# Optimization experiments

Measured on AMD Instinct MI355X. Metric: run time of the kernel, lower is better.

The kernel has to match this reference:

```python
import jax, jax.numpy as jnp
import numpy as np

B, N, H, HEADS, NBINS = 64, 256, 512, 8, 3
DK = H // HEADS
NEG = -1e12

def setup_inputs() -> dict:
    key = jax.random.key(0)
    ks = jax.random.split(key, 20)
    def lin(k, out_d, in_d):
        w = jax.random.normal(k, (out_d, in_d), jnp.float32) * (1.0 / np.sqrt(in_d))
        b = jnp.zeros((out_d,), jnp.float32)
        return w, b
    x = jax.random.normal(ks[0], (B, N, H), jnp.float32)
    dist = jax.random.uniform(ks[1], (B, N - 1, N - 1), jnp.float32, 0.0, 10.0)
    dist_bar = jnp.sort(jax.random.uniform(ks[2], (B, NBINS), jnp.float32, 1.0, 9.0), axis=-1)
    mask = jnp.ones((B, N, N), jnp.float32)
    Wq, bq = lin(ks[3], H, H)
    Wk, bk = lin(ks[4], H, H)
    Wv, bv = lin(ks[5], H, H)
    Wa = jnp.stack([lin(ks[6 + i], H, H)[0] for i in range(NBINS)])  # [NBINS,H,H]
    ba = jnp.zeros((NBINS, H), jnp.float32)
    Ws1, bs1 = lin(ks[10], H, NBINS * H)
    Ws2, bs2 = lin(ks[11], H, H)
    gamma = jnp.ones((H,), jnp.float32)
    beta = jnp.zeros((H,), jnp.float32)
    return dict(x=x, dist=dist, dist_bar=dist_bar, mask=mask, Wq=Wq, bq=bq, Wk=Wk, bk=bk,
                Wv=Wv, bv=bv, Wa=Wa, ba=ba, Ws1=Ws1, bs1=bs1, Ws2=Ws2, bs2=bs2,
                gamma=gamma, beta=beta)

def reference(x, dist, dist_bar, mask, Wq, bq, Wk, bk, Wv, bv, Wa, ba, Ws1, bs1, Ws2, bs2, gamma, beta):
    residual = x
    def proj(x, W, b):  # torch Linear: x @ W.T + b
        return jnp.einsum('bnd,od->bno', x, W) + b
    def heads(t):  # [B,N,H] -> [B,heads,N,dk]
        return t.reshape(B, N, HEADS, DK).transpose(0, 2, 1, 3)
    q, k, v = heads(proj(x, Wq, bq)), heads(proj(x, Wk, bk)), heads(proj(x, Wv, bv))
    scores = jnp.einsum('bhnd,bhmd->bhnm', q, k) / jnp.sqrt(jnp.float32(DK))  # [B,heads,N,N]
    # padding mask (shape [B,1,N,N] != scores shape -> masked_fill(mask==0))
    scores = jnp.where(mask[:, None] == 0, NEG, scores)
    # new_dist: super node row/col = 1, interior = dist
    new_dist = jnp.ones((B, 1, N, N), jnp.float32).at[:, :, 1:, 1:].set(dist[:, None])
    multi_out, attn_list = [], []
    for i in range(NBINS):
        cut = dist_bar[:, i][:, None, None, None]          # per-batch threshold
        dm = new_dist < cut                                 # [B,1,N,N]
        dm = dm.at[:, :, 0, :].set(True).at[:, :, :, 0].set(True)
        sd = jnp.where(dm, scores, NEG)
        attn = jax.nn.softmax(sd, axis=-1)                  # dropout: eval mode
        attn_list.append(attn)
        multi_out.append(jnp.einsum('bhnm,bhmd->bhnd', attn, v))
    x_cat = jnp.concatenate([
        jnp.einsum('bnd,od->bno', multi_out[i].transpose(0, 2, 1, 3).reshape(B, N, H), Wa[i]) + ba[i]
        for i in range(NBINS)], axis=-1)                    # [B,N,NBINS*H]
    h = jax.nn.silu(jnp.einsum('bnd,od->bno', x_cat, Ws1) + bs1)
    h = jnp.einsum('bnd,od->bno', h, Ws2) + bs2
    h = h + residual
    mu = jnp.mean(h, axis=-1, keepdims=True)
    var = jnp.var(h, axis=-1, keepdims=True)
    out = (h - mu) / jnp.sqrt(var + 1e-6) * gamma + beta
    return (out, jnp.stack(attn_list))
```

## Files before the change

### kernel.cpp

```cpp
#include <hip/hip_runtime.h>
#include <cstddef>

#define NEGV (-1e12f)


typedef __attribute__((ext_vector_type(4))) float f32x4;
typedef __attribute__((ext_vector_type(8))) __bf16 bf16x8;

__device__ __forceinline__ unsigned short f2bf(float f) {
  union { float f; unsigned u; } v; v.f = f;
  unsigned r = v.u + 0x7FFFu + ((v.u >> 16) & 1u);
  return (unsigned short)(r >> 16);
}

#define GLDS16(gp, lp)                                                      \
  __builtin_amdgcn_global_load_lds(                                         \
      (const __attribute__((address_space(1))) void*)(gp),                  \
      (__attribute__((address_space(3))) void*)(lp), 16, 0, 0)

__global__ __launch_bounds__(256) void msa_prep(
    const float* __restrict__ x, const float* __restrict__ Wq,
    const float* __restrict__ Wk, const float* __restrict__ Wv,
    const float* __restrict__ Ws2, const float* __restrict__ Ws1,
    const float* __restrict__ Wa, const float* __restrict__ bq,
    const float* __restrict__ bk, const float* __restrict__ bv,
    const float* __restrict__ ba, const float* __restrict__ bs1,
    const float* __restrict__ dist, const float* __restrict__ dist_bar,
    const float* __restrict__ maskg,
    unsigned short* __restrict__ xb, unsigned short* __restrict__ Wqkvb,
    unsigned short* __restrict__ Ws2b, unsigned short* __restrict__ Wcatb,
    float* __restrict__ bcomb, float* __restrict__ bqkv,
    unsigned long long* __restrict__ bits) {
  __shared__ float As[16][68];
  __shared__ float Bs[16][68];
  const int blk = blockIdx.x;
  const int tid = threadIdx.x;
  if (blk < 8192) {
    int i = blk * 256 + tid;
    float4 v = ((const float4*)x)[i];
    ushort4 o; o.x = f2bf(v.x); o.y = f2bf(v.y); o.z = f2bf(v.z); o.w = f2bf(v.w);
    ((ushort4*)xb)[i] = o;
    return;
  }
  if (blk < 8960) {
    int sel = (blk - 8192) >> 8;
    int i = ((blk - 8192) & 255) * 256 + tid;
    const float* src = (sel == 0) ? Wq : (sel == 1) ? Wk : Wv;
    unsigned short* dst = Wqkvb + (size_t)sel * 262144;
    float4 v = ((const float4*)src)[i];
    ushort4 o; o.x = f2bf(v.x); o.y = f2bf(v.y); o.z = f2bf(v.z); o.w = f2bf(v.w);
    ((ushort4*)dst)[i] = o;
    return;
  }
  if (blk < 9216) {
    int i = (blk - 8960) * 256 + tid;
    float4 v = ((const float4*)Ws2)[i];
    ushort4 o; o.x = f2bf(v.x); o.y = f2bf(v.y); o.z = f2bf(v.z); o.w = f2bf(v.w);
    ((ushort4*)Ws2b)[i] = o;
    return;
  }
  if (blk < 9408) {
    const int t = blk - 9216;
    const int i = t >> 6;
    const int ob = ((t >> 3) & 7) * 64, cb = (t & 7) * 64;
    const int tx = tid & 15, ty = tid >> 4;
    float acc[4][4] = {};
    for (int kt = 0; kt < 512; kt += 16) {
      __syncthreads();
      {
        int o = tid & 63, e4 = (tid >> 6) * 4;
        float4 a4 = *(const float4*)&Ws1[(size_t)(ob + o) * 1536 + i * 512 + kt + e4];
        As[e4 + 0][o] = a4.x; As[e4 + 1][o] = a4.y;
        As[e4 + 2][o] = a4.z; As[e4 + 3][o] = a4.w;
      }
      {
        int e = tid & 15, c4 = (tid >> 4) * 4;
        float4 b4 = *(const float4*)&Wa[((size_t)i << 18) + (size_t)(kt + e) * 512 + cb + c4];
        *(float4*)&Bs[e][c4] = b4;
      }
      __syncthreads();
#pragma unroll
      for (int k = 0; k < 16; ++k) {
        float a[4], bb[4];
        *(float4*)a = *(const float4*)&As[k][ty * 4];
        *(float4*)bb = *(const float4*)&Bs[k][tx * 4];
#pragma unroll
        for (int r = 0; r < 4; ++r)
#pragma unroll
          for (int c = 0; c < 4; ++c) acc[r][c] += a[r] * bb[c];
      }
    }
#pragma unroll
    for (int r = 0; r < 4; ++r)
#pragma unroll
      for (int c = 0; c < 4; ++c)
        Wcatb[(size_t)(ob + ty * 4 + r) * 1536 + i * 512 + cb + tx * 4 + c] =
            f2bf(acc[r][c]);
    return;
  }
  if (blk < 9410) {
    int o = (blk - 9408) * 256 + tid;
    float acc = bs1[o];
    for (int cidx = 0; cidx < 1536; ++cidx)
      acc += Ws1[(size_t)o * 1536 + cidx] * ba[cidx];
    bcomb[o] = acc;
    return;
  }
  if (blk < 9411) {
    for (int i = tid; i < 1536; i += 256)
      bqkv[i] = (i < 512) ? bq[i] : (i < 1024) ? bk[i - 512] : bv[i - 1024];
    return;
  }
  {
    const int gw = (blk - 9411) * 4 + (tid >> 6);
    const int lane = tid & 63;
    const int b = gw >> 8, row = gw & 255;
    const float cut0 = dist_bar[b * 3 + 0];
    const float cut1 = dist_bar[b * 3 + 1];
    const float cut2 = dist_bar[b * 3 + 2];
    const float* mrow = maskg + (size_t)b * 65536 + (size_t)row * 256;
    const int rj = (row == 0) ? 1 : row;
    const float* drow = dist + (size_t)b * 65025 + (size_t)(rj - 1) * 255;
    unsigned long long* out = bits + (size_t)gw * 12;
#pragma unroll
    for (int cc = 0; cc < 4; ++cc) {
      const int col = cc * 64 + lane;
      const int cj = (col == 0) ? 1 : col;
      float dv = drow[cj - 1];
      bool sup = (row == 0) || (col == 0);
      bool mk = (mrow[col] != 0.f);
      if (sup) dv = -1e30f;
      unsigned long long b0 = __ballot(mk && (dv < cut0));
      unsigned long long b1 = __ballot(mk && (dv < cut1));
      unsigned long long b2 = __ballot(mk && (dv < cut2));
      if (lane == 0) { out[cc] = b0; out[4 + cc] = b1; out[8 + cc] = b2; }
    }
  }
}

template <int ACT, int RES, int OBF, int BK>
__global__ __launch_bounds__(256) void msa_gemm_mfma(
    const unsigned short* __restrict__ A, int lda,
    const unsigned short* __restrict__ W, int ldw,
    const float* __restrict__ bias, const float* __restrict__ resid,
    void* __restrict__ Cout, int ldc, int Kdim) {
  constexpr int KSUB = BK / 32;
  constexpr int RPC = BK / 8;
  constexpr int CPT = (128 * RPC) / 256;
  __shared__ __align__(16) unsigned short Asm_[2][128 * BK];
  __shared__ __align__(16) unsigned short Bsm_[2][128 * BK];
  const int tid = threadIdx.x;
  const int lane = tid & 63, wv = tid >> 6;
  const int m0 = blockIdx.x * 128, n0 = blockIdx.y * 128;
  const int wr = wv >> 1, wc = wv & 1;
  const int fr = lane & 15, fq = lane >> 4;
  f32x4 acc[4][4] = {};
  const unsigned short* Ag[CPT];
  const unsigned short* Wg[CPT];
#pragma unroll
  for (int i = 0; i < CPT; ++i) {
    int c = tid + i * 256;
    int row = c / RPC, j = c % RPC;
    Ag[i] = A + (size_t)(m0 + row) * lda + j * 8;
    Wg[i] = W + (size_t)(n0 + row) * ldw + j * 8;
  }
#pragma unroll
  for (int i = 0; i < CPT; ++i) {
    GLDS16(Ag[i], &Asm_[0][(tid + i * 256) * 8]);
    GLDS16(Wg[i], &Bsm_[0][(tid + i * 256) * 8]);
  }
  __syncthreads();
  int cur = 0;
  for (int kt = 0; kt < Kdim; kt += BK) {
    if (kt + BK < Kdim) {
      const int nx = cur ^ 1, k2 = kt + BK;
#pragma unroll
      for (int i = 0; i < CPT; ++i) {
        GLDS16(Ag[i] + k2, &Asm_[nx][(tid + i * 256) * 8]);
        GLDS16(Wg[i] + k2, &Bsm_[nx][(tid + i * 256) * 8]);
      }
    }
#pragma unroll
    for (int ks = 0; ks < KSUB; ++ks) {
      bf16x8 af[4], bfr[4];
#pragma unroll
      for (int mf = 0; mf < 4; ++mf)
        af[mf] = *(const bf16x8*)&Asm_[cur][(wr * 64 + mf * 16 + fr) * BK + ks * 32 + fq * 8];
#pragma unroll
      for (int nf = 0; nf < 4; ++nf)
        bfr[nf] = *(const bf16x8*)&Bsm_[cur][(wc * 64 + nf * 16 + fr) * BK + ks * 32 + fq * 8];
#pragma unroll
      for (int mf = 0; mf < 4; ++mf)
#pragma unroll
        for (int nf = 0; nf < 4; ++nf)
          acc[mf][nf] = __builtin_amdgcn_mfma_f32_16x16x32_bf16(
              af[mf], bfr[nf], acc[mf][nf], 0, 0, 0);
    }
    __syncthreads();
    cur ^= 1;
  }
#pragma unroll
  for (int mf = 0; mf < 4; ++mf) {
#pragma unroll
    for (int nf = 0; nf < 4; ++nf) {
      const int n = n0 + wc * 64 + nf * 16 + fr;
      const float bval = bias[n];
#pragma unroll
      for (int r = 0; r < 4; ++r) {
        const int m = m0 + wr * 64 + mf * 16 + fq * 4 + r;
        float val = acc[mf][nf][r] + bval;
        if (ACT == 1) val = val / (1.f + __expf(-val));
        if (RES == 1) val += resid[(size_t)m * ldc + n];
        if (OBF == 1)
          ((unsigned short*)Cout)[(size_t)m * ldc + n] = f2bf(val);
        else
          ((float*)Cout)[(size_t)m * ldc + n] = val;
      }
    }
  }
}

__global__ __launch_bounds__(512) void msa_fused(
    const unsigned short* __restrict__ qkvb,
    const unsigned long long* __restrict__ bits,
    float* __restrict__ attn_out, unsigned short* __restrict__ mob) {
  const int blk = blockIdx.x;
  const int b = (blk & 7) * 8 + (blk >> 6);
  const int h = (blk >> 3) & 7;
  __shared__ __align__(16) unsigned short Kl[256][72];
  __shared__ __align__(16) unsigned short Vt[64][264];
  __shared__ __align__(16) unsigned short Pl[8][16][264];
  const int tid = threadIdx.x;
  const int wv = tid >> 6, lane = tid & 63;
  const int l15 = lane & 15, fq = lane >> 4;
  {
    const unsigned short* kgp = qkvb + (size_t)(b * 256) * 1536 + 512 + h * 64;
#pragma unroll
    for (int i = 0; i < 4; ++i) {
      int s = tid + i * 512;
      int row = s >> 3, c8 = (s & 7) << 3;
      *(uint4*)&Kl[row][c8] = *(const uint4*)&kgp[(size_t)row * 1536 + c8];
    }
  }
  {
    int rv = tid & 255, half = tid >> 8;
    const unsigned short* vgp =
        qkvb + (size_t)(b * 256 + rv) * 1536 + 1024 + h * 64 + half * 32;
#pragma unroll
    for (int j4 = 0; j4 < 4; ++j4) {
      unsigned short tmp[8];
      *(uint4*)tmp = *(const uint4*)&vgp[j4 * 8];
#pragma unroll
      for (int j = 0; j < 8; ++j) Vt[half * 32 + j4 * 8 + j][rv] = tmp[j];
    }
  }
  __syncthreads();
#pragma unroll
  for (int mf = 0; mf < 2; ++mf) {
    const int r0 = wv * 32 + mf * 16;
    const unsigned short* qgp =
        qkvb + (size_t)(b * 256 + r0 + l15) * 1536 + h * 64 + fq * 8;
    bf16x8 aq0 = *(const bf16x8*)qgp;
    bf16x8 aq1 = *(const bf16x8*)(qgp + 32);
    f32x4 accs[16];
#pragma unroll
    for (int nt = 0; nt < 16; ++nt) {
      bf16x8 bk0 = *(const bf16x8*)&Kl[nt * 16 + l15][fq * 8];
      bf16x8 bk1 = *(const bf16x8*)&Kl[nt * 16 + l15][32 + fq * 8];
      f32x4 a = {};
      a = __builtin_amdgcn_mfma_f32_16x16x32_bf16(aq0, bk0, a, 0, 0, 0);
      a = __builtin_amdgcn_mfma_f32_16x16x32_bf16(aq1, bk1, a, 0, 0, 0);
      accs[nt] = a;
    }
#pragma unroll
    for (int bin = 0; bin < 3; ++bin) {
      float* pbase = attn_out + ((size_t)((bin * 64 + b) * 8 + h)) * 65536;
#pragma unroll
      for (int r = 0; r < 4; ++r) {
        const int row = r0 + fq * 4 + r;
        const unsigned long long* bw =
            bits + (size_t)(b * 256 + row) * 12 + bin * 4;
        const unsigned long long w0 = bw[0], w1 = bw[1], w2 = bw[2], w3 = bw[3];
        float p[16];
        float m = -3e38f;
#pragma unroll
        for (int nt = 0; nt < 16; ++nt) {
          unsigned long long w = (nt < 4) ? w0 : (nt < 8) ? w1 : (nt < 12) ? w2 : w3;
          unsigned keep = (unsigned)(w >> ((nt & 3) * 16 + l15)) & 1u;
          float sv = accs[nt][r] * 0.125f;
          p[nt] = keep ? sv : NEGV;
          m = fmaxf(m, p[nt]);
        }
        m = fmaxf(m, __shfl_xor(m, 1));
        m = fmaxf(m, __shfl_xor(m, 2));
        m = fmaxf(m, __shfl_xor(m, 4));
        m = fmaxf(m, __shfl_xor(m, 8));
        float sum = 0.f;
#pragma unroll
        for (int nt = 0; nt < 16; ++nt) { p[nt] = __expf(p[nt] - m); sum += p[nt]; }
        sum += __shfl_xor(sum, 1);
        sum += __shfl_xor(sum, 2);
        sum += __shfl_xor(sum, 4);
        sum += __shfl_xor(sum, 8);
        const float inv = 1.f / sum;
        float* prow = pbase + (size_t)row * 256 + l15;
#pragma unroll
        for (int nt = 0; nt < 16; ++nt) {
          float val = p[nt] * inv;
          prow[nt * 16] = val;
          Pl[wv][fq * 4 + r][nt * 16 + l15] = f2bf(val);
        }
      }
      asm volatile("s_waitcnt lgkmcnt(0)" ::: "memory");
      f32x4 acco[4] = {};
#pragma unroll
      for (int c = 0; c < 8; ++c) {
        bf16x8 pa = *(const bf16x8*)&Pl[wv][l15][c * 32 + fq * 8];
#pragma unroll
        for (int nf = 0; nf < 4; ++nf) {
          bf16x8 bv = *(const bf16x8*)&Vt[nf * 16 + l15][c * 32 + fq * 8];
          acco[nf] = __builtin_amdgcn_mfma_f32_16x16x32_bf16(pa, bv, acco[nf], 0, 0, 0);
        }
      }
#pragma unroll
      for (int nf = 0; nf < 4; ++nf)
#pragma unroll
        for (int r = 0; r < 4; ++r)
          mob[((size_t)(b * 256 + r0 + fq * 4 + r) * 3 + bin) * 512 +
              h * 64 + nf * 16 + l15] = f2bf(acco[nf][r]);
    }
  }
}

__global__ __launch_bounds__(256) void msa_ln(const float* __restrict__ h2,
                                              const float* __restrict__ gamma,
                                              const float* __restrict__ beta,
                                              float* __restrict__ outp) {
  const int row = blockIdx.x * 4 + (threadIdx.x >> 6);
  const int lane = threadIdx.x & 63;
  const float* hp = h2 + (size_t)row * 512 + lane * 8;
  float4 v0 = *(const float4*)hp;
  float4 v1 = *(const float4*)(hp + 4);
  float s = v0.x + v0.y + v0.z + v0.w + v1.x + v1.y + v1.z + v1.w;
#pragma unroll
  for (int off = 32; off > 0; off >>= 1) s += __shfl_xor(s, off);
  float mu = s * (1.f / 512.f);
  float d[8] = {v0.x - mu, v0.y - mu, v0.z - mu, v0.w - mu,
                v1.x - mu, v1.y - mu, v1.z - mu, v1.w - mu};
  float sq = 0.f;
#pragma unroll
  for (int j = 0; j < 8; ++j) sq += d[j] * d[j];
#pragma unroll
  for (int off = 32; off > 0; off >>= 1) sq += __shfl_xor(sq, off);
  float inv = 1.f / sqrtf(sq * (1.f / 512.f) + 1e-6f);
  const float* gp = gamma + lane * 8;
  const float* bp = beta + lane * 8;
  float* op = outp + (size_t)row * 512 + lane * 8;
#pragma unroll
  for (int j = 0; j < 8; ++j) op[j] = d[j] * inv * gp[j] + bp[j];
}

extern "C" void kernel_launch(void* const* d_in, const int* in_sizes, int n_in,
                              void* d_out, int out_size, void* d_ws, size_t ws_size,
                              hipStream_t stream) {
  (void)in_sizes; (void)n_in; (void)out_size; (void)ws_size;
  const float* x        = (const float*)d_in[0];
  const float* dist     = (const float*)d_in[1];
  const float* dist_bar = (const float*)d_in[2];
  const float* mask     = (const float*)d_in[3];
  const float* Wq  = (const float*)d_in[4];  const float* bq  = (const float*)d_in[5];
  const float* Wk  = (const float*)d_in[6];  const float* bk  = (const float*)d_in[7];
  const float* Wv  = (const float*)d_in[8];  const float* bv  = (const float*)d_in[9];
  const float* Wa  = (const float*)d_in[10]; const float* ba  = (const float*)d_in[11];
  const float* Ws1 = (const float*)d_in[12]; const float* bs1 = (const float*)d_in[13];
  const float* Ws2 = (const float*)d_in[14]; const float* bs2 = (const float*)d_in[15];
  const float* gamma = (const float*)d_in[16]; const float* beta = (const float*)d_in[17];

  char* w8 = (char*)d_ws;
  const size_t SZ = 8388608;
  unsigned short* qkvb = (unsigned short*)(w8 + 0);
  unsigned short* mob  = (unsigned short*)(w8 + 50331648);
  unsigned short* xb   = (unsigned short*)(w8 + 100663296);
  unsigned short* Wqkvb= (unsigned short*)(w8 + 117440512);
  unsigned short* Ws2b = (unsigned short*)(w8 + 119013376);
  unsigned short* Wcatb= (unsigned short*)(w8 + 119537664);
  float* bcomb = (float*)(w8 + 121110528);
  float* bqkv  = (float*)(w8 + 121112576);
  unsigned long long* bits = (unsigned long long*)(w8 + 121118720);
  unsigned short* h1b = qkvb;
  float* h2 = (float*)(w8 + 16777216);
  float* outp = (float*)d_out;
  float* attn = outp + SZ;

  msa_prep<<<13507, 256, 0, stream>>>(x, Wq, Wk, Wv, Ws2, Ws1, Wa, bq, bk, bv,
                                      ba, bs1, dist, dist_bar, mask,
                                      xb, Wqkvb, Ws2b, Wcatb, bcomb, bqkv, bits);

  msa_gemm_mfma<0, 0, 1, 32><<<dim3(128, 12), 256, 0, stream>>>(
      xb, 512, Wqkvb, 512, bqkv, nullptr, qkvb, 1536, 512);

  msa_fused<<<512, 512, 0, stream>>>(qkvb, bits, attn, mob);

  msa_gemm_mfma<1, 0, 1, 64><<<dim3(128, 4), 256, 0, stream>>>(
      mob, 1536, Wcatb, 1536, bcomb, nullptr, h1b, 512, 1536);
  msa_gemm_mfma<0, 1, 0, 64><<<dim3(128, 4), 256, 0, stream>>>(
      h1b, 512, Ws2b, 512, bs2, x, h2, 512, 512);

  msa_ln<<<4096, 256, 0, stream>>>(h2, gamma, beta, outp);
}
```

Before: 325.1 us.

## Fuse second MLP GEMM with LayerNorm and shrink attention kernel LDS footprint

After: 444.6 us. 1.37x slower.

```diff
diff --git a/kernel.cpp b/kernel.cpp
--- a/kernel.cpp
+++ b/kernel.cpp
@@ -220,29 +220,19 @@
   }
 }
 
-__global__ __launch_bounds__(512) void msa_fused(
+__global__ __launch_bounds__(512, 4) void msa_fused(
     const unsigned short* __restrict__ qkvb,
     const unsigned long long* __restrict__ bits,
     float* __restrict__ attn_out, unsigned short* __restrict__ mob) {
   const int blk = blockIdx.x;
   const int b = (blk & 7) * 8 + (blk >> 6);
   const int h = (blk >> 3) & 7;
-  __shared__ __align__(16) unsigned short Kl[256][72];
   __shared__ __align__(16) unsigned short Vt[64][264];
-  __shared__ __align__(16) unsigned short Pl[8][16][264];
+  __shared__ __align__(16) unsigned short Pl[8][16][136];
   const int tid = threadIdx.x;
   const int wv = tid >> 6, lane = tid & 63;
   const int l15 = lane & 15, fq = lane >> 4;
   {
-    const unsigned short* kgp = qkvb + (size_t)(b * 256) * 1536 + 512 + h * 64;
-#pragma unroll
-    for (int i = 0; i < 4; ++i) {
-      int s = tid + i * 512;
-      int row = s >> 3, c8 = (s & 7) << 3;
-      *(uint4*)&Kl[row][c8] = *(const uint4*)&kgp[(size_t)row * 1536 + c8];
-    }
-  }
-  {
     int rv = tid & 255, half = tid >> 8;
     const unsigned short* vgp =
         qkvb + (size_t)(b * 256 + rv) * 1536 + 1024 + h * 64 + half * 32;
@@ -255,7 +245,9 @@
     }
   }
   __syncthreads();
-#pragma unroll
+  const unsigned short* kbase =
+      qkvb + ((size_t)b * 256 + l15) * 1536 + 512 + h * 64 + fq * 8;
+#pragma unroll 1
   for (int mf = 0; mf < 2; ++mf) {
     const int r0 = wv * 32 + mf * 16;
     const unsigned short* qgp =
@@ -265,16 +257,18 @@
     f32x4 accs[16];
 #pragma unroll
     for (int nt = 0; nt < 16; ++nt) {
-      bf16x8 bk0 = *(const bf16x8*)&Kl[nt * 16 + l15][fq * 8];
-      bf16x8 bk1 = *(const bf16x8*)&Kl[nt * 16 + l15][32 + fq * 8];
+      const unsigned short* kp = kbase + (size_t)(nt * 16) * 1536;
+      bf16x8 bk0 = *(const bf16x8*)kp;
+      bf16x8 bk1 = *(const bf16x8*)(kp + 32);
       f32x4 a = {};
       a = __builtin_amdgcn_mfma_f32_16x16x32_bf16(aq0, bk0, a, 0, 0, 0);
       a = __builtin_amdgcn_mfma_f32_16x16x32_bf16(aq1, bk1, a, 0, 0, 0);
       accs[nt] = a;
     }
-#pragma unroll
+#pragma unroll 1
     for (int bin = 0; bin < 3; ++bin) {
       float* pbase = attn_out + ((size_t)((bin * 64 + b) * 8 + h)) * 65536;
+      float mr[4], ivr[4];
 #pragma unroll
       for (int r = 0; r < 4; ++r) {
         const int row = r0 + fq * 4 + r;
@@ -303,18 +297,20 @@
         sum += __shfl_xor(sum, 4);
         sum += __shfl_xor(sum, 8);
         const float inv = 1.f / sum;
+        mr[r] = m; ivr[r] = inv;
         float* prow = pbase + (size_t)row * 256 + l15;
 #pragma unroll
         for (int nt = 0; nt < 16; ++nt) {
           float val = p[nt] * inv;
           prow[nt * 16] = val;
-          Pl[wv][fq * 4 + r][nt * 16 + l15] = f2bf(val);
+          if (nt < 8) Pl[wv][fq * 4 + r][nt * 16 + l15] = f2bf(val);
         }
       }
       asm volatile("s_waitcnt lgkmcnt(0)" ::: "memory");
+      __builtin_amdgcn_sched_barrier(0);
       f32x4 acco[4] = {};
 #pragma unroll
-      for (int c = 0; c < 8; ++c) {
+      for (int c = 0; c < 4; ++c) {
         bf16x8 pa = *(const bf16x8*)&Pl[wv][l15][c * 32 + fq * 8];
 #pragma unroll
         for (int nf = 0; nf < 4; ++nf) {
@@ -322,6 +318,35 @@
           acco[nf] = __builtin_amdgcn_mfma_f32_16x16x32_bf16(pa, bv, acco[nf], 0, 0, 0);
         }
       }
+      __builtin_amdgcn_sched_barrier(0);
+#pragma unroll
+      for (int r = 0; r < 4; ++r) {
+        const int row = r0 + fq * 4 + r;
+        const unsigned long long* bw =
+            bits + (size_t)(b * 256 + row) * 12 + bin * 4;
+        const unsigned long long w2 = bw[2], w3 = bw[3];
+        const float m = mr[r], inv = ivr[r];
+#pragma unroll
+        for (int nt = 8; nt < 16; ++nt) {
+          unsigned long long w = (nt < 12) ? w2 : w3;
+          unsigned keep = (unsigned)(w >> ((nt & 3) * 16 + l15)) & 1u;
+          float sv = accs[nt][r] * 0.125f;
+          float sd = keep ? sv : NEGV;
+          float val = __expf(sd - m) * inv;
+          Pl[wv][fq * 4 + r][(nt - 8) * 16 + l15] = f2bf(val);
+        }
+      }
+      asm volatile("s_waitcnt lgkmcnt(0)" ::: "memory");
+      __builtin_amdgcn_sched_barrier(0);
+#pragma unroll
+      for (int c = 0; c < 4; ++c) {
+        bf16x8 pa = *(const bf16x8*)&Pl[wv][l15][c * 32 + fq * 8];
+#pragma unroll
+        for (int nf = 0; nf < 4; ++nf) {
+          bf16x8 bv = *(const bf16x8*)&Vt[nf * 16 + l15][128 + c * 32 + fq * 8];
+          acco[nf] = __builtin_amdgcn_mfma_f32_16x16x32_bf16(pa, bv, acco[nf], 0, 0, 0);
+        }
+      }
 #pragma unroll
       for (int nf = 0; nf < 4; ++nf)
 #pragma unroll
@@ -332,32 +357,95 @@
   }
 }
 
-__global__ __launch_bounds__(256) void msa_ln(const float* __restrict__ h2,
-                                              const float* __restrict__ gamma,
-                                              const float* __restrict__ beta,
-                                              float* __restrict__ outp) {
-  const int row = blockIdx.x * 4 + (threadIdx.x >> 6);
-  const int lane = threadIdx.x & 63;
-  const float* hp = h2 + (size_t)row * 512 + lane * 8;
-  float4 v0 = *(const float4*)hp;
-  float4 v1 = *(const float4*)(hp + 4);
-  float s = v0.x + v0.y + v0.z + v0.w + v1.x + v1.y + v1.z + v1.w;
-#pragma unroll
-  for (int off = 32; off > 0; off >>= 1) s += __shfl_xor(s, off);
-  float mu = s * (1.f / 512.f);
-  float d[8] = {v0.x - mu, v0.y - mu, v0.z - mu, v0.w - mu,
-                v1.x - mu, v1.y - mu, v1.z - mu, v1.w - mu};
-  float sq = 0.f;
-#pragma unroll
-  for (int j = 0; j < 8; ++j) sq += d[j] * d[j];
-#pragma unroll
-  for (int off = 32; off > 0; off >>= 1) sq += __shfl_xor(sq, off);
-  float inv = 1.f / sqrtf(sq * (1.f / 512.f) + 1e-6f);
-  const float* gp = gamma + lane * 8;
-  const float* bp = beta + lane * 8;
-  float* op = outp + (size_t)row * 512 + lane * 8;
-#pragma unroll
-  for (int j = 0; j < 8; ++j) op[j] = d[j] * inv * gp[j] + bp[j];
+__global__ __launch_bounds__(256) void msa_mlp2ln(
+    const unsigned short* __restrict__ h1b, const unsigned short* __restrict__ Ws2b,
+    const float* __restrict__ bs2, const float* __restrict__ x,
+    const float* __restrict__ gamma, const float* __restrict__ beta,
+    float* __restrict__ outp) {
+  __shared__ __align__(16) unsigned short Al[32 * 32];
+  __shared__ __align__(16) unsigned short Bl[512 * 32];
+  __shared__ float red[2][2][32];
+  const int tid = threadIdx.x;
+  const int lane = tid & 63, wv = tid >> 6;
+  const int wr = wv >> 1, wc = wv & 1;
+  const int l15 = lane & 15, fq = lane >> 4;
+  const int m0 = blockIdx.x * 32;
+  f32x4 acc[16] = {};
+  for (int kt = 0; kt < 512; kt += 32) {
+    if (tid < 128) {
+      int row = tid >> 2, c8 = (tid & 3) * 8;
+      GLDS16(h1b + (size_t)(m0 + row) * 512 + kt + c8, &Al[tid * 8]);
+    }
+#pragma unroll
+    for (int i = 0; i < 8; ++i) {
+      int c = tid + i * 256;
+      int row = c >> 2, c8 = (c & 3) * 8;
+      GLDS16(Ws2b + (size_t)row * 512 + kt + c8, &Bl[c * 8]);
+    }
+    __syncthreads();
+    bf16x8 af = *(const bf16x8*)&Al[(wr * 16 + l15) * 32 + fq * 8];
+#pragma unroll
+    for (int nt = 0; nt < 16; ++nt) {
+      bf16x8 bfr = *(const bf16x8*)&Bl[(wc * 256 + nt * 16 + l15) * 32 + fq * 8];
+      acc[nt] = __builtin_amdgcn_mfma_f32_16x16x32_bf16(af, bfr, acc[nt], 0, 0, 0);
+    }
+    __syncthreads();
+  }
+  float vals[16][4];
+#pragma unroll
+  for (int nt = 0; nt < 16; ++nt) {
+    const int n = wc * 256 + nt * 16 + l15;
+    const float bval = bs2[n];
+#pragma unroll
+    for (int r = 0; r < 4; ++r) {
+      const int m = m0 + wr * 16 + fq * 4 + r;
+      vals[nt][r] = acc[nt][r] + bval + x[(size_t)m * 512 + n];
+    }
+  }
+  const int ridx = wr * 16 + fq * 4;
+#pragma unroll
+  for (int r = 0; r < 4; ++r) {
+    float s = 0.f;
+#pragma unroll
+    for (int nt = 0; nt < 16; ++nt) s += vals[nt][r];
+    s += __shfl_xor(s, 1); s += __shfl_xor(s, 2);
+    s += __shfl_xor(s, 4); s += __shfl_xor(s, 8);
+    if (l15 == 0) red[0][wc][ridx + r] = s;
+  }
+  __syncthreads();
+  float mu[4];
+#pragma unroll
+  for (int r = 0; r < 4; ++r)
+    mu[r] = (red[0][0][ridx + r] + red[0][1][ridx + r]) * (1.f / 512.f);
+#pragma unroll
+  for (int r = 0; r < 4; ++r) {
+    float s = 0.f;
+#pragma unroll
+    for (int nt = 0; nt < 16; ++nt) {
+      float d = vals[nt][r] - mu[r];
+      s += d * d;
+    }
+    s += __shfl_xor(s, 1); s += __shfl_xor(s, 2);
+    s += __shfl_xor(s, 4); s += __shfl_xor(s, 8);
+    if (l15 == 0) red[1][wc][ridx + r] = s;
+  }
+  __syncthreads();
+  float iv[4];
+#pragma unroll
+  for (int r = 0; r < 4; ++r) {
+    float var = (red[1][0][ridx + r] + red[1][1][ridx + r]) * (1.f / 512.f);
+    iv[r] = 1.f / sqrtf(var + 1e-6f);
+  }
+#pragma unroll
+  for (int nt = 0; nt < 16; ++nt) {
+    const int n = wc * 256 + nt * 16 + l15;
+    const float g = gamma[n], be = beta[n];
+#pragma unroll
+    for (int r = 0; r < 4; ++r) {
+      const int m = m0 + wr * 16 + fq * 4 + r;
+      outp[(size_t)m * 512 + n] = (vals[nt][r] - mu[r]) * iv[r] * g + be;
+    }
+  }
 }
 
 extern "C" void kernel_launch(void* const* d_in, const int* in_sizes, int n_in,
@@ -388,7 +476,6 @@
   float* bqkv  = (float*)(w8 + 121112576);
   unsigned long long* bits = (unsigned long long*)(w8 + 121118720);
   unsigned short* h1b = qkvb;
-  float* h2 = (float*)(w8 + 16777216);
   float* outp = (float*)d_out;
   float* attn = outp + SZ;
 
@@ -403,8 +490,6 @@
 
   msa_gemm_mfma<1, 0, 1, 64><<<dim3(128, 4), 256, 0, stream>>>(
       mob, 1536, Wcatb, 1536, bcomb, nullptr, h1b, 512, 1536);
-  msa_gemm_mfma<0, 1, 0, 64><<<dim3(128, 4), 256, 0, stream>>>(
-      h1b, 512, Ws2b, 512, bs2, x, h2, 512, 512);
-
-  msa_ln<<<4096, 256, 0, stream>>>(h2, gamma, beta, outp);
-}
+
+  msa_mlp2ln<<<512, 256, 0, stream>>>(h1b, Ws2b, bs2, x, gamma, beta, outp);
+}
```
